# Performance work log

Hardware: AMD Instinct MI355X
Metric: run time of the kernel (lower is better)

## Reference

```python
import jax, jax.numpy as jnp
import numpy as np

N, C, R, T, H, W = 2, 256, 8, 4, 32, 32
CK = C // R  # key channels = 32


def setup_inputs() -> dict:
    key = jax.random.key(0)
    ks = jax.random.split(key, 10)
    s = 0.05  # small init so dual softmax is not saturated
    return {
        "x1": jax.random.normal(ks[0], (N, C, T, H, W), jnp.float32),
        "x2": jax.random.normal(ks[1], (N, C, T, H, W), jnp.float32),
        "Wk1": jax.random.normal(ks[2], (CK, C), jnp.float32) * s,
        "bk1": jax.random.normal(ks[3], (CK,), jnp.float32) * s,
        "Wk2": jax.random.normal(ks[4], (CK, C), jnp.float32) * s,
        "bk2": jax.random.normal(ks[5], (CK,), jnp.float32) * s,
        "Wv1": jax.random.normal(ks[6], (C, C), jnp.float32) * s,
        "bv1": jax.random.normal(ks[7], (C,), jnp.float32) * s,
        "Wv2": jax.random.normal(ks[8], (C, C), jnp.float32) * s,
        "bv2": jax.random.normal(ks[9], (C,), jnp.float32) * s,
    }


def reference(x1, x2, Wk1, bk1, Wk2, bk2, Wv1, bv1, Wv2, bv2):
    n, c, t, h, w = x1.shape
    L = t * h * w
    x1f = x1.reshape(n, c, L)  # [n, C, L]
    x2f = x2.reshape(n, c, L)
    # 1x1x1 Conv3d == per-position channel mixing
    k1 = jnp.einsum('kc,ncl->nkl', Wk1, x1f) + bk1[None, :, None]  # [n, CK, L]
    k2 = jnp.einsum('kc,ncl->nkl', Wk2, x2f) + bk2[None, :, None]
    v1 = jnp.einsum('dc,ncl->ndl', Wv1, x1f) + bv1[None, :, None]  # [n, C, L]
    v2 = jnp.einsum('dc,ncl->ndl', Wv2, x2f) + bv2[None, :, None]
    # cor[n, l, m] = sum_k k1[n,k,l] * k2[n,k,m]
    cor = jnp.einsum('nkl,nkm->nlm', k1, k2)  # [n, L, L]
    attn1 = jax.nn.softmax(cor, axis=2)  # rows normalized
    attn2 = jax.nn.softmax(cor, axis=1)  # cols normalized
    r1 = jnp.einsum('ncl,nlm->ncm', v1, attn1).reshape(n, c, t, h, w)
    r2 = jnp.einsum('ncm,nlm->ncl', v2, attn2).reshape(n, c, t, h, w)
    return (x1 + r1, x2 + r2)
```

## Files before the change

### kernel.cpp

```cpp
#include <hip/hip_runtime.h>
#include <hip/hip_bf16.h>

#define N_  2
#define C_  256
#define CK_ 32
#define L_  4096

typedef __attribute__((ext_vector_type(8))) short short8;
typedef __attribute__((ext_vector_type(4))) float f32x4;
typedef __attribute__((ext_vector_type(2))) unsigned int uint2v;
typedef unsigned short ushort;

__device__ __forceinline__ ushort f2bf(float f){
  unsigned u = __float_as_uint(f);
  u += 0x7fffu + ((u >> 16) & 1u);
  return (ushort)(u >> 16);
}

__device__ __forceinline__ f32x4 mfma16(short8 a, short8 b, f32x4 c){
  return __builtin_amdgcn_mfma_f32_16x16x32_bf16(a, b, c, 0, 0, 0);
}

__global__ __launch_bounds__(256) void convert_x_kernel(
    const float* __restrict__ x1, const float* __restrict__ x2,
    ushort* __restrict__ xT1, ushort* __restrict__ xT2){
  __shared__ float tt[64][130];
  int z = blockIdx.z; int n = z & 1;
  const float* x = (z >> 1) ? x2 : x1;
  ushort* xT = (z >> 1) ? xT2 : xT1;
  int l0 = blockIdx.x * 64, c0 = blockIdx.y * 128;
  int t = threadIdx.x;
  const float* xs = x + (size_t)n * C_ * L_;
  ushort* xd = xT + (size_t)n * L_ * C_;
  int lq = (t & 15) * 4, cl = t >> 4;
#pragma unroll
  for (int r = 0; r < 8; ++r){
    int c = r * 16 + cl;
    float4 f = *(const float4*)(xs + (size_t)(c0 + c) * L_ + l0 + lq);
    tt[lq + 0][c] = f.x; tt[lq + 1][c] = f.y; tt[lq + 2][c] = f.z; tt[lq + 3][c] = f.w;
  }
  __syncthreads();
  int c8 = (t & 15) * 8, ll = t >> 4;
#pragma unroll
  for (int r = 0; r < 4; ++r){
    int l = r * 16 + ll;
    union { ushort u[8]; short8 v; } pk;
#pragma unroll
    for (int j = 0; j < 8; ++j) pk.u[j] = f2bf(tt[l][c8 + j]);
    *(short8*)(xd + (size_t)(l0 + l) * C_ + c0 + c8) = pk.v;
  }
}

__global__ __launch_bounds__(256) void convert_w_kernel(
    const float* __restrict__ Wk1, const float* __restrict__ Wk2,
    const float* __restrict__ Wv1, const float* __restrict__ Wv2,
    ushort* __restrict__ o1, ushort* __restrict__ o2,
    ushort* __restrict__ o3, ushort* __restrict__ o4){
  int idx = blockIdx.x * 256 + threadIdx.x;
  const int KS = CK_ * C_;
  const int VS = C_ * C_;
  if (idx < KS)                 o1[idx] = f2bf(Wk1[idx]);
  else if (idx < 2*KS)          o2[idx - KS] = f2bf(Wk2[idx - KS]);
  else if (idx < 2*KS + VS)     o3[idx - 2*KS] = f2bf(Wv1[idx - 2*KS]);
  else if (idx < 2*KS + 2*VS)   o4[idx - 2*KS - VS] = f2bf(Wv2[idx - 2*KS - VS]);
}

__global__ __launch_bounds__(256) void proj_kernel(
    const ushort* __restrict__ xT1, const ushort* __restrict__ xT2,
    const ushort* __restrict__ Wk1b, const ushort* __restrict__ Wk2b,
    const ushort* __restrict__ Wv1b, const ushort* __restrict__ Wv2b,
    const float* __restrict__ bk1, const float* __restrict__ bk2,
    const float* __restrict__ bv1, const float* __restrict__ bv2,
    ushort* __restrict__ k1t, ushort* __restrict__ k2t,
    ushort* __restrict__ v1,  ushort* __restrict__ v2){
  int y = blockIdx.y, n = blockIdx.z;
  int t = threadIdx.x, w = t >> 6, lane = t & 63, quad = lane >> 4, low = lane & 15;
  const ushort* X; const ushort* W; const float* bias; ushort* outp; int jt; bool isK;
  if (y < 8)       { X = xT1; W = Wv1b; bias = bv1; outp = v1;  jt = y;     isK = false; }
  else if (y < 16) { X = xT2; W = Wv2b; bias = bv2; outp = v2;  jt = y - 8; isK = false; }
  else if (y == 16){ X = xT1; W = Wk1b; bias = bk1; outp = k1t; jt = 0;     isK = true; }
  else             { X = xT2; W = Wk2b; bias = bk2; outp = k2t; jt = 0;     isK = true; }
  int j0 = jt * 32;
  int l0 = blockIdx.x * 128 + w * 32;
  const ushort* Xn = X + (size_t)n * L_ * C_;
  f32x4 acc[2][2] = {};
#pragma unroll
  for (int kc = 0; kc < 8; ++kc){
    short8 a[2], b[2];
#pragma unroll
    for (int js = 0; js < 2; ++js)
      a[js] = *(const short8*)(W + (size_t)(j0 + js*16 + low)*C_ + kc*32 + quad*8);
#pragma unroll
    for (int ls = 0; ls < 2; ++ls)
      b[ls] = *(const short8*)(Xn + (size_t)(l0 + ls*16 + low)*C_ + kc*32 + quad*8);
#pragma unroll
    for (int js = 0; js < 2; ++js)
#pragma unroll
      for (int ls = 0; ls < 2; ++ls)
        acc[js][ls] = mfma16(a[js], b[ls], acc[js][ls]);
  }
#pragma unroll
  for (int js = 0; js < 2; ++js){
    f32x4 bb = *(const f32x4*)(bias + j0 + js*16 + quad*4);
#pragma unroll
    for (int ls = 0; ls < 2; ++ls){
      int l = l0 + ls*16 + low;
      if (!isK){
#pragma unroll
        for (int r = 0; r < 4; ++r){
          int j = j0 + js*16 + quad*4 + r;
          outp[((size_t)n*C_ + j)*L_ + l] = f2bf(acc[js][ls][r] + bb[r]);
        }
      } else {
        union { ushort u[4]; uint2v v; } pk;
#pragma unroll
        for (int r = 0; r < 4; ++r) pk.u[r] = f2bf(acc[js][ls][r] + bb[r]);
        *(uint2v*)(outp + ((size_t)n*L_ + l)*CK_ + j0 + js*16 + quad*4) = pk.v;
      }
    }
  }
}

__global__ __launch_bounds__(256) void stats_kernel(
    const ushort* __restrict__ k1t, const ushort* __restrict__ k2t,
    float* __restrict__ S1part, float* __restrict__ S2part){
  int n = blockIdx.z;
  int m0 = blockIdx.x * 128, l0 = blockIdx.y * 128;
  int t = threadIdx.x, w = t >> 6, lane = t & 63, quad = lane >> 4, low = lane & 15;
  __shared__ float rowsum[128];
  __shared__ float colsum[4][128];
  const ushort* ka = k1t + (size_t)n * L_ * CK_;
  const ushort* kb = k2t + (size_t)n * L_ * CK_;
  short8 a[2], b[8];
#pragma unroll
  for (int lt = 0; lt < 2; ++lt)
    a[lt] = *(const short8*)(ka + (size_t)(l0 + w*32 + lt*16 + low)*CK_ + quad*8);
#pragma unroll
  for (int mt = 0; mt < 8; ++mt)
    b[mt] = *(const short8*)(kb + (size_t)(m0 + mt*16 + low)*CK_ + quad*8);
  float rp[2][4] = {}; float cp[8] = {};
  const f32x4 zero = {0.f, 0.f, 0.f, 0.f};
#pragma unroll
  for (int lt = 0; lt < 2; ++lt)
#pragma unroll
    for (int mt = 0; mt < 8; ++mt){
      f32x4 e = mfma16(a[lt], b[mt], zero);
#pragma unroll
      for (int r = 0; r < 4; ++r){
        float v = __builtin_amdgcn_exp2f(e[r] * 1.44269504088896f);
        rp[lt][r] += v;
        cp[mt] += v;
      }
    }
#pragma unroll
  for (int lt = 0; lt < 2; ++lt)
#pragma unroll
    for (int r = 0; r < 4; ++r){
      float v = rp[lt][r];
      v += __shfl_xor(v, 1); v += __shfl_xor(v, 2);
      v += __shfl_xor(v, 4); v += __shfl_xor(v, 8);
      if (low == 0) rowsum[w*32 + lt*16 + quad*4 + r] = v;
    }
#pragma unroll
  for (int mt = 0; mt < 8; ++mt){
    float v = cp[mt];
    v += __shfl_xor(v, 16); v += __shfl_xor(v, 32);
    if (quad == 0) colsum[w][mt*16 + low] = v;
  }
  __syncthreads();
  if (t < 128)
    S1part[((size_t)n*32 + blockIdx.x)*L_ + l0 + t] = rowsum[t];
  else {
    int m = t - 128;
    S2part[((size_t)n*32 + blockIdx.y)*L_ + m0 + m] =
        colsum[0][m] + colsum[1][m] + colsum[2][m] + colsum[3][m];
  }
}

__global__ __launch_bounds__(256) void reduce_inv_kernel(
    const float* __restrict__ S1part, const float* __restrict__ S2part,
    float* __restrict__ invS1, float* __restrict__ invS2){
  int idx = blockIdx.x * 256 + threadIdx.x;
  int which = idx >> 13;
  int r = idx & 8191;
  int n = r >> 12, l = r & 4095;
  const float* P = which ? S2part : S1part;
  float s = 0.f;
#pragma unroll
  for (int j = 0; j < 32; ++j) s += P[((size_t)n*32 + j)*L_ + l];
  (which ? invS2 : invS1)[(size_t)n*L_ + l] = -__builtin_amdgcn_logf(s);
}

#define LOG2E_ 1.44269504088896f

__device__ __forceinline__ void e_phase(ushort (*buf)[144],
    short8 a0, short8 a1, f32x4 s0, f32x4 s1, const short8* be,
    int w, int quad, int low){
  const f32x4 zero = {0.f, 0.f, 0.f, 0.f};
#pragma unroll
  for (int ps = 0; ps < 2; ++ps){
    short8 a = ps ? a1 : a0;
    f32x4 sv = ps ? s1 : s0;
#pragma unroll
    for (int qs = 0; qs < 4; ++qs){
      f32x4 e = mfma16(a, be[qs], zero);
      float p0 = __builtin_amdgcn_exp2f(__fmaf_rn(e[0], LOG2E_, sv[0]));
      float p1 = __builtin_amdgcn_exp2f(__fmaf_rn(e[1], LOG2E_, sv[1]));
      float p2 = __builtin_amdgcn_exp2f(__fmaf_rn(e[2], LOG2E_, sv[2]));
      float p3 = __builtin_amdgcn_exp2f(__fmaf_rn(e[3], LOG2E_, sv[3]));
      union { __hip_bfloat162 h[2]; uint2v v; } pk;
      pk.h[0] = __float22bfloat162_rn(make_float2(p0, p1));
      pk.h[1] = __float22bfloat162_rn(make_float2(p2, p3));
      *(uint2v*)&buf[qs*16 + low][w*32 + ps*16 + quad*4] = pk.v;
    }
  }
}

__device__ __forceinline__ void main_phase(const ushort (*buf)[144],
    const short8* v, f32x4 (*acc)[4], int quad, int low){
#pragma unroll
  for (int ks = 0; ks < 4; ++ks){
    short8 bb[4];
#pragma unroll
    for (int qs = 0; qs < 4; ++qs)
      bb[qs] = *(const short8*)&buf[qs*16 + low][ks*32 + quad*8];
#pragma unroll
    for (int cs = 0; cs < 2; ++cs)
#pragma unroll
      for (int qs = 0; qs < 4; ++qs)
        acc[cs][qs] = mfma16(v[ks*2 + cs], bb[qs], acc[cs][qs]);
  }
}

__global__ __launch_bounds__(256, 2) void cross_attn_r_kernel(
    const ushort* __restrict__ k1t, const ushort* __restrict__ k2t,
    const ushort* __restrict__ v1,  const ushort* __restrict__ v2,
    const float* __restrict__ invS1, const float* __restrict__ invS2,
    const float* __restrict__ x1, const float* __restrict__ x2,
    float* __restrict__ out){
  int z = blockIdx.z; int which = z >> 1; int n = z & 1;
  const ushort* kA = which ? k2t : k1t;
  const ushort* kB = which ? k1t : k2t;
  const ushort* V  = which ? v2  : v1;
  const float* iS  = which ? invS2 : invS1;
  const float* X   = which ? x2 : x1;
  float* O = out + (size_t)which * N_ * C_ * L_;
  int q0 = blockIdx.x * 64, c0 = blockIdx.y * 128;
  int t = threadIdx.x, w = t >> 6, lane = t & 63, quad = lane >> 4, low = lane & 15;
  __shared__ __align__(16) ushort ptile[2][64][144];
  const ushort* kAn = kA + (size_t)n * L_ * CK_;
  const ushort* kBn = kB + (size_t)n * L_ * CK_;
  const ushort* Vn  = V  + (size_t)n * C_ * L_;
  const float*  iSn = iS + (size_t)n * L_;

  const ushort* kA_base = kAn + (size_t)(w*32 + low) * CK_ + quad * 8;
  const float*  sv_base = iSn + w*32 + quad * 4;
  const ushort* V_base  = Vn + (size_t)(c0 + w*32 + low) * L_ + quad * 8;

  short8 be[4];
#pragma unroll
  for (int qs = 0; qs < 4; ++qs)
    be[qs] = *(const short8*)(kBn + (size_t)(q0 + qs*16 + low) * CK_ + quad * 8);

  f32x4 acc[2][4] = {};

  short8 a0A, a1A, a0B, a1B;
  f32x4  s0A, s1A, s0B, s1B;
  short8 vA[8], vB[8];

#define LOAD_SET(A0, A1, S0, S1, VV, P) do{                                   \
    A0 = *(const short8*)(kA_base + (size_t)(P) * CK_);                       \
    A1 = *(const short8*)(kA_base + (size_t)((P) + 16) * CK_);                \
    S0 = *(const f32x4*)(sv_base + (P));                                      \
    S1 = *(const f32x4*)(sv_base + (P) + 16);                                 \
    VV[0] = *(const short8*)(V_base + (P) + 0*32);                            \
    VV[2] = *(const short8*)(V_base + (P) + 1*32);                            \
    VV[4] = *(const short8*)(V_base + (P) + 2*32);                            \
    VV[6] = *(const short8*)(V_base + (P) + 3*32);                            \
    VV[1] = *(const short8*)(V_base + (size_t)16*L_ + (P) + 0*32);            \
    VV[3] = *(const short8*)(V_base + (size_t)16*L_ + (P) + 1*32);            \
    VV[5] = *(const short8*)(V_base + (size_t)16*L_ + (P) + 2*32);            \
    VV[7] = *(const short8*)(V_base + (size_t)16*L_ + (P) + 3*32);            \
  }while(0)

  LOAD_SET(a0A, a1A, s0A, s1A, vA, 0);

  for (int kk = 0; kk < L_ / 256; ++kk){
    int pB  = (2*kk + 1) * 128;
    int pA2 = ((2*kk + 2) & 31) * 128;
    e_phase(ptile[0], a0A, a1A, s0A, s1A, be, w, quad, low);
    LOAD_SET(a0B, a1B, s0B, s1B, vB, pB);
    __syncthreads();
    main_phase(ptile[0], vA, acc, quad, low);
    e_phase(ptile[1], a0B, a1B, s0B, s1B, be, w, quad, low);
    LOAD_SET(a0A, a1A, s0A, s1A, vA, pA2);
    __syncthreads();
    main_phase(ptile[1], vB, acc, quad, low);
  }
#undef LOAD_SET

#pragma unroll
  for (int cs = 0; cs < 2; ++cs)
#pragma unroll
    for (int qs = 0; qs < 4; ++qs){
      int cb = c0 + w*32 + cs*16 + quad*4;
      int q = q0 + qs*16 + low;
#pragma unroll
      for (int r = 0; r < 4; ++r){
        size_t idx = ((size_t)n * C_ + cb + r) * L_ + q;
        O[idx] = X[idx] + acc[cs][qs][r];
      }
    }
}

extern "C" void kernel_launch(void* const* d_in, const int* in_sizes, int n_in,
                              void* d_out, int out_size, void* d_ws, size_t ws_size,
                              hipStream_t stream) {
  const float* x1  = (const float*)d_in[0];
  const float* x2  = (const float*)d_in[1];
  const float* Wk1 = (const float*)d_in[2];
  const float* bk1 = (const float*)d_in[3];
  const float* Wk2 = (const float*)d_in[4];
  const float* bk2 = (const float*)d_in[5];
  const float* Wv1 = (const float*)d_in[6];
  const float* bv1 = (const float*)d_in[7];
  const float* Wv2 = (const float*)d_in[8];
  const float* bv2 = (const float*)d_in[9];

  char* ws = (char*)d_ws;
  size_t off = 0;
  auto carve = [&](size_t bytes) -> void* {
    void* p = ws + off; off += (bytes + 255) & ~(size_t)255; return p;
  };
  ushort* xT1   = (ushort*)carve((size_t)N_*L_*C_*2);
  ushort* xT2   = (ushort*)carve((size_t)N_*L_*C_*2);
  ushort* Wk1b  = (ushort*)carve((size_t)CK_*C_*2);
  ushort* Wk2b  = (ushort*)carve((size_t)CK_*C_*2);
  ushort* Wv1b  = (ushort*)carve((size_t)C_*C_*2);
  ushort* Wv2b  = (ushort*)carve((size_t)C_*C_*2);
  ushort* k1t   = (ushort*)carve((size_t)N_*L_*CK_*2);
  ushort* k2t   = (ushort*)carve((size_t)N_*L_*CK_*2);
  ushort* v1    = (ushort*)carve((size_t)N_*C_*L_*2);
  ushort* v2    = (ushort*)carve((size_t)N_*C_*L_*2);
  float*  S1p   = (float*)carve((size_t)N_*32*L_*4);
  float*  S2p   = (float*)carve((size_t)N_*32*L_*4);
  float*  invS1 = (float*)carve((size_t)N_*L_*4);
  float*  invS2 = (float*)carve((size_t)N_*L_*4);

  convert_x_kernel<<<dim3(L_/64, C_/128, 4), 256, 0, stream>>>(x1, x2, xT1, xT2);
  convert_w_kernel<<<dim3((2*CK_*C_ + 2*C_*C_) / 256), 256, 0, stream>>>(
      Wk1, Wk2, Wv1, Wv2, Wk1b, Wk2b, Wv1b, Wv2b);
  proj_kernel<<<dim3(L_/128, 18, N_), 256, 0, stream>>>(
      xT1, xT2, Wk1b, Wk2b, Wv1b, Wv2b, bk1, bk2, bv1, bv2, k1t, k2t, v1, v2);
  stats_kernel<<<dim3(L_/128, L_/128, N_), 256, 0, stream>>>(k1t, k2t, S1p, S2p);
  reduce_inv_kernel<<<dim3(2*N_*L_/256), 256, 0, stream>>>(S1p, S2p, invS1, invS2);
  cross_attn_r_kernel<<<dim3(L_/64, C_/128, 2*N_), 256, 0, stream>>>(
      k1t, k2t, v1, v2, invS1, invS2, x1, x2, (float*)d_out);
}
```

Before: 197.5 us.

## Keep softmax probabilities in registers and split key dimension across warps

The attention kernel no longer writes exp probabilities to shared memory for the PV matmul. Each warp now computes its own 32-key slice of probabilities and feeds them straight from registers as MFMA B operands, relying on a row permutation of the key loads so the accumulator layout matches the operand layout. Every warp covers all 128 channels over a disjoint key range, and the four partial accumulators are summed through shared memory in the epilogue, which also writes float4 outputs. This removes the per-iteration LDS traffic and barriers, at the cost of 128 accumulator registers per thread, possible occupancy pressure, and an epilogue reduction with 16 barriers.

```diff
diff --git a/kernel.cpp b/kernel.cpp
--- a/kernel.cpp
+++ b/kernel.cpp
@@ -193,45 +193,6 @@
 
 #define LOG2E_ 1.44269504088896f
 
-__device__ __forceinline__ void e_phase(ushort (*buf)[144],
-    short8 a0, short8 a1, f32x4 s0, f32x4 s1, const short8* be,
-    int w, int quad, int low){
-  const f32x4 zero = {0.f, 0.f, 0.f, 0.f};
-#pragma unroll
-  for (int ps = 0; ps < 2; ++ps){
-    short8 a = ps ? a1 : a0;
-    f32x4 sv = ps ? s1 : s0;
-#pragma unroll
-    for (int qs = 0; qs < 4; ++qs){
-      f32x4 e = mfma16(a, be[qs], zero);
-      float p0 = __builtin_amdgcn_exp2f(__fmaf_rn(e[0], LOG2E_, sv[0]));
-      float p1 = __builtin_amdgcn_exp2f(__fmaf_rn(e[1], LOG2E_, sv[1]));
-      float p2 = __builtin_amdgcn_exp2f(__fmaf_rn(e[2], LOG2E_, sv[2]));
-      float p3 = __builtin_amdgcn_exp2f(__fmaf_rn(e[3], LOG2E_, sv[3]));
-      union { __hip_bfloat162 h[2]; uint2v v; } pk;
-      pk.h[0] = __float22bfloat162_rn(make_float2(p0, p1));
-      pk.h[1] = __float22bfloat162_rn(make_float2(p2, p3));
-      *(uint2v*)&buf[qs*16 + low][w*32 + ps*16 + quad*4] = pk.v;
-    }
-  }
-}
-
-__device__ __forceinline__ void main_phase(const ushort (*buf)[144],
-    const short8* v, f32x4 (*acc)[4], int quad, int low){
-#pragma unroll
-  for (int ks = 0; ks < 4; ++ks){
-    short8 bb[4];
-#pragma unroll
-    for (int qs = 0; qs < 4; ++qs)
-      bb[qs] = *(const short8*)&buf[qs*16 + low][ks*32 + quad*8];
-#pragma unroll
-    for (int cs = 0; cs < 2; ++cs)
-#pragma unroll
-      for (int qs = 0; qs < 4; ++qs)
-        acc[cs][qs] = mfma16(v[ks*2 + cs], bb[qs], acc[cs][qs]);
-  }
-}
-
 __global__ __launch_bounds__(256, 2) void cross_attn_r_kernel(
     const ushort* __restrict__ k1t, const ushort* __restrict__ k2t,
     const ushort* __restrict__ v1,  const ushort* __restrict__ v2,
@@ -247,70 +208,82 @@
   float* O = out + (size_t)which * N_ * C_ * L_;
   int q0 = blockIdx.x * 64, c0 = blockIdx.y * 128;
   int t = threadIdx.x, w = t >> 6, lane = t & 63, quad = lane >> 4, low = lane & 15;
-  __shared__ __align__(16) ushort ptile[2][64][144];
+  __shared__ __align__(16) float red[4][16][68];
   const ushort* kAn = kA + (size_t)n * L_ * CK_;
   const ushort* kBn = kB + (size_t)n * L_ * CK_;
   const ushort* Vn  = V  + (size_t)n * C_ * L_;
   const float*  iSn = iS + (size_t)n * L_;
 
-  const ushort* kA_base = kAn + (size_t)(w*32 + low) * CK_ + quad * 8;
-  const float*  sv_base = iSn + w*32 + quad * 4;
-  const ushort* V_base  = Vn + (size_t)(c0 + w*32 + low) * L_ + quad * 8;
+  const ushort* kA_base = kAn + (size_t)((low >> 2) * 8 + (low & 3)) * CK_ + quad * 8;
+  const float*  sv_base = iSn + quad * 8;
+  const ushort* V_base  = Vn + (size_t)(c0 + low) * L_ + quad * 8;
 
   short8 be[4];
 #pragma unroll
   for (int qs = 0; qs < 4; ++qs)
     be[qs] = *(const short8*)(kBn + (size_t)(q0 + qs*16 + low) * CK_ + quad * 8);
 
-  f32x4 acc[2][4] = {};
-
-  short8 a0A, a1A, a0B, a1B;
-  f32x4  s0A, s1A, s0B, s1B;
-  short8 vA[8], vB[8];
-
-#define LOAD_SET(A0, A1, S0, S1, VV, P) do{                                   \
-    A0 = *(const short8*)(kA_base + (size_t)(P) * CK_);                       \
-    A1 = *(const short8*)(kA_base + (size_t)((P) + 16) * CK_);                \
-    S0 = *(const f32x4*)(sv_base + (P));                                      \
-    S1 = *(const f32x4*)(sv_base + (P) + 16);                                 \
-    VV[0] = *(const short8*)(V_base + (P) + 0*32);                            \
-    VV[2] = *(const short8*)(V_base + (P) + 1*32);                            \
-    VV[4] = *(const short8*)(V_base + (P) + 2*32);                            \
-    VV[6] = *(const short8*)(V_base + (P) + 3*32);                            \
-    VV[1] = *(const short8*)(V_base + (size_t)16*L_ + (P) + 0*32);            \
-    VV[3] = *(const short8*)(V_base + (size_t)16*L_ + (P) + 1*32);            \
-    VV[5] = *(const short8*)(V_base + (size_t)16*L_ + (P) + 2*32);            \
-    VV[7] = *(const short8*)(V_base + (size_t)16*L_ + (P) + 3*32);            \
-  }while(0)
-
-  LOAD_SET(a0A, a1A, s0A, s1A, vA, 0);
-
-  for (int kk = 0; kk < L_ / 256; ++kk){
-    int pB  = (2*kk + 1) * 128;
-    int pA2 = ((2*kk + 2) & 31) * 128;
-    e_phase(ptile[0], a0A, a1A, s0A, s1A, be, w, quad, low);
-    LOAD_SET(a0B, a1B, s0B, s1B, vB, pB);
+  f32x4 acc[8][4] = {};
+  const f32x4 zero = {0.f, 0.f, 0.f, 0.f};
+
+  int pfirst = w * 32;
+  short8 a0 = *(const short8*)(kA_base + (size_t)pfirst * CK_);
+  short8 a1 = *(const short8*)(kA_base + (size_t)(pfirst + 4) * CK_);
+  f32x4 sv0 = *(const f32x4*)(sv_base + pfirst);
+  f32x4 sv1 = *(const f32x4*)(sv_base + pfirst + 4);
+
+  for (int kk = 0; kk < L_ / 128; ++kk){
+    int p = kk * 128 + w * 32;
+    short8 vv[8];
+#pragma unroll
+    for (int ct = 0; ct < 8; ++ct)
+      vv[ct] = *(const short8*)(V_base + (size_t)ct * 16 * L_ + p);
+    short8 pb[4];
+#pragma unroll
+    for (int qs = 0; qs < 4; ++qs){
+      f32x4 e0 = mfma16(a0, be[qs], zero);
+      f32x4 e1 = mfma16(a1, be[qs], zero);
+      union { ushort u[8]; short8 v; } pk;
+#pragma unroll
+      for (int r = 0; r < 4; ++r)
+        pk.u[r]     = f2bf(__builtin_amdgcn_exp2f(__fmaf_rn(e0[r], LOG2E_, sv0[r])));
+#pragma unroll
+      for (int r = 0; r < 4; ++r)
+        pk.u[4 + r] = f2bf(__builtin_amdgcn_exp2f(__fmaf_rn(e1[r], LOG2E_, sv1[r])));
+      pb[qs] = pk.v;
+    }
+    int pn = ((kk + 1) & 31) * 128 + w * 32;
+    a0 = *(const short8*)(kA_base + (size_t)pn * CK_);
+    a1 = *(const short8*)(kA_base + (size_t)(pn + 4) * CK_);
+    sv0 = *(const f32x4*)(sv_base + pn);
+    sv1 = *(const f32x4*)(sv_base + pn + 4);
+#pragma unroll
+    for (int ct = 0; ct < 8; ++ct)
+#pragma unroll
+      for (int qs = 0; qs < 4; ++qs)
+        acc[ct][qs] = mfma16(vv[ct], pb[qs], acc[ct][qs]);
+  }
+
+  int cl = t >> 4, qg = (t & 15) * 4;
+#pragma unroll
+  for (int ct = 0; ct < 8; ++ct){
+#pragma unroll
+    for (int qs = 0; qs < 4; ++qs)
+#pragma unroll
+      for (int r = 0; r < 4; ++r)
+        red[w][quad*4 + r][qs*16 + low] = acc[ct][qs][r];
     __syncthreads();
-    main_phase(ptile[0], vA, acc, quad, low);
-    e_phase(ptile[1], a0B, a1B, s0B, s1B, be, w, quad, low);
-    LOAD_SET(a0A, a1A, s0A, s1A, vA, pA2);
+    f32x4 s0 = *(const f32x4*)&red[0][cl][qg];
+    f32x4 s1 = *(const f32x4*)&red[1][cl][qg];
+    f32x4 s2 = *(const f32x4*)&red[2][cl][qg];
+    f32x4 s3 = *(const f32x4*)&red[3][cl][qg];
+    f32x4 s = (s0 + s1) + (s2 + s3);
+    size_t idx = ((size_t)n * C_ + c0 + ct*16 + cl) * L_ + q0 + qg;
+    const float4 xv = *(const float4*)(X + idx);
+    float4 o = make_float4(xv.x + s[0], xv.y + s[1], xv.z + s[2], xv.w + s[3]);
+    *(float4*)(O + idx) = o;
     __syncthreads();
-    main_phase(ptile[1], vB, acc, quad, low);
-  }
-#undef LOAD_SET
-
-#pragma unroll
-  for (int cs = 0; cs < 2; ++cs)
-#pragma unroll
-    for (int qs = 0; qs < 4; ++qs){
-      int cb = c0 + w*32 + cs*16 + quad*4;
-      int q = q0 + qs*16 + low;
-#pragma unroll
-      for (int r = 0; r < 4; ++r){
-        size_t idx = ((size_t)n * C_ + cb + r) * L_ + q;
-        O[idx] = X[idx] + acc[cs][qs][r];
-      }
-    }
+  }
 }
 
 extern "C" void kernel_launch(void* const* d_in, const int* in_sizes, int n_in,
```

After: 199.8 us. Within noise of the previous version (+1.2%).
